# Optimization experiments

Measured on AMD Instinct MI355X. Metric: run time of the kernel, lower is better.

## Reference

```python
import jax, jax.numpy as jnp
import numpy as np

B = 262144
IN = 12
HID = 256
OUT = 12


def setup_inputs() -> dict:
    key = jax.random.key(0)
    ks = jax.random.split(key, 7)
    def lin(k, fan_in, fan_out):
        kw, kb = jax.random.split(k)
        bound = 1.0 / np.sqrt(fan_in)
        W = jax.random.uniform(kw, (fan_in, fan_out), jnp.float32, -bound, bound)
        b = jax.random.uniform(kb, (fan_out,), jnp.float32, -bound, bound)
        return W, b
    W1, b1 = lin(ks[0], IN, HID)
    W2, b2 = lin(ks[1], HID, HID)
    W3, b3 = lin(ks[2], HID, OUT)
    inp = jax.random.normal(ks[3], (B, IN), jnp.float32)
    return {"inp": inp, "W1": W1, "b1": b1, "W2": W2, "b2": b2, "W3": W3, "b3": b3}


def _forward(inp, W1, b1, W2, b2, W3, b3):
    h = jax.nn.relu(inp @ W1 + b1)
    h = jax.nn.relu(h @ W2 + b2)
    x = h @ W3 + b3  # [B, 12]

    pos = jnp.tanh(x[:, 0:3])
    vel = jnp.tanh(x[:, 3:6])
    pts = jax.nn.sigmoid(x[:, 6:7])
    clus = jnp.tanh(x[:, 7:10])
    sun = jnp.tanh(x[:, 10:12])

    # position clipped to unit sphere
    dist = jnp.linalg.norm(pos, axis=1, keepdims=True)  # [B,1]
    pos_c = jnp.where(dist > 1.0, pos / dist, pos)

    # inspected points: over-estimates set to 1, under-estimates set to previous
    prev = inp[:, 6:7]
    pts_c = jnp.where(pts > 1.0, 1.0, pts)
    pts_c = jnp.where(pts < prev, prev, pts_c)

    # cluster: push away from deputy if moving toward it, then clip to unit sphere
    delta = clus - inp[:, 7:10]
    deputy = inp[:, 0:3] - inp[:, 7:10]
    nd = deputy / jnp.linalg.norm(deputy, axis=1, keepdims=True)
    dd = jnp.einsum('ij,ij->i', delta, deputy)[:, None]  # [B,1]
    offset = jnp.where(dd > 0.0, clus - nd, clus)
    cdist = jnp.linalg.norm(offset, axis=1, keepdims=True)
    # NOTE: non-exceeding rows keep the ORIGINAL tanh prediction (torch semantics)
    clus_c = jnp.where(cdist > 1.0, offset / cdist, clus)

    # sun angle projected onto unit circle
    sun_c = sun / jnp.linalg.norm(sun, axis=1, keepdims=True)

    return jnp.concatenate([pos_c, vel, pts_c, clus_c, sun_c], axis=1)


def reference(inp, W1, b1, W2, b2, W3, b3):
    return _forward(inp, W1, b1, W2, b2, W3, b3)
```

## Files before the change

### kernel.cpp

```cpp
#include <hip/hip_runtime.h>
#include <math.h>

#define NIN 12
#define HID 256
#define NOUT 12
#define BM 64
#define NBLK (262144 / BM)

typedef _Float16 f16;
typedef f16 f16x8 __attribute__((ext_vector_type(8)));
typedef float f32x4 __attribute__((ext_vector_type(4)));

__device__ __forceinline__ void gll16(const void* g, void* l) {
    __builtin_amdgcn_global_load_lds(
        (const __attribute__((address_space(1))) unsigned int*)g,
        (__attribute__((address_space(3))) unsigned int*)l, 16, 0, 0);
}

__global__ void prep_w2(const float* __restrict__ W2, f16* __restrict__ w2p) {
    const int e = (blockIdx.x * 256 + threadIdx.x) * 4;
    const int k = e >> 8, col0 = e & 255;
    const float4 w = *(const float4*)(W2 + k * HID + col0);
    const int s = k >> 5, lgw = (k >> 3) & 3, j = k & 7;
    #pragma unroll
    for (int q = 0; q < 4; ++q) {
        const float v = ((const float*)&w)[q];
        const f16 hi = (f16)v;
        const f16 lo = (f16)(v - (float)hi);
        const int c = col0 + q, ct = c >> 4, cc = c & 15, l = (lgw << 4) | cc;
        w2p[(size_t)(((s*2 + 0)*16 + ct)*64 + l)*8 + j] = hi;
        w2p[(size_t)(((s*2 + 1)*16 + ct)*64 + l)*8 + j] = lo;
    }
}

__global__ __launch_bounds__(256, 3)
void mlp_main(const float* __restrict__ inp, const float* __restrict__ W1,
              const float* __restrict__ b1, const float* __restrict__ W2,
              const float* __restrict__ b2, const float* __restrict__ W3,
              const float* __restrict__ b3, const f16* __restrict__ w2p,
              float* __restrict__ out)
{
    __shared__ __align__(16) unsigned char smem[48896];
    __shared__ int nflag;
    __shared__ int flaglist[16];

    f16*   Bl   = (f16*)smem;
    float* W3s  = (float*)(smem + 32768);
    float* b2s  = (float*)(smem + 45056);
    float* h1f  = (float*)(smem + 46080);
    float* h2f  = (float*)(smem + 47104);
    float* psum = (float*)(smem + 48128);

    const int t    = threadIdx.x;
    const int lane = t & 63;
    const int wid  = t >> 6;
    const int cl   = lane & 15;
    const int lg   = lane >> 4;
    const int row0 = blockIdx.x * BM;

    if (t == 0) nflag = 0;

    {
        const char* w3c = (const char*)W3;
        #pragma unroll
        for (int i = 0; i < 3; ++i) {
            const int off = (wid*3 + i) * 1024;
            gll16(w3c + off + lane*16, (char*)W3s + off);
        }
        if (wid == 0) gll16((const char*)b2 + lane*16, (char*)b2s);
    }

    const int myrow = row0 + wid*16 + cl;
    float xin[12];
    {
        const f32x4* ip = (const f32x4*)(inp + (size_t)myrow * NIN);
        const f32x4 a = ip[0], b = ip[1], c = ip[2];
        xin[0]=a.x; xin[1]=a.y; xin[2]=a.z; xin[3]=a.w;
        xin[4]=b.x; xin[5]=b.y; xin[6]=b.z; xin[7]=b.w;
        xin[8]=c.x; xin[9]=c.y; xin[10]=c.z; xin[11]=c.w;
    }

    f32x4 acc[16];
    {
        const f32x4 zero = {0.f, 0.f, 0.f, 0.f};
        #pragma unroll
        for (int ct = 0; ct < 16; ++ct) acc[ct] = zero;
    }
    for (int s = 0; s < 8; ++s) {
        __syncthreads();
        const char* src = (const char*)w2p + (size_t)s * 32768;
        #pragma unroll
        for (int i = 0; i < 8; ++i) {
            const int off = (i*4 + wid) * 1024;
            gll16(src + off + lane*16, (char*)Bl + off);
        }
        const int k0 = 32*s + 8*lg;
        float a0[8];
        {
            const f32x4 bb0 = *(const f32x4*)(b1 + k0);
            const f32x4 bb1 = *(const f32x4*)(b1 + k0 + 4);
            a0[0]=bb0.x; a0[1]=bb0.y; a0[2]=bb0.z; a0[3]=bb0.w;
            a0[4]=bb1.x; a0[5]=bb1.y; a0[6]=bb1.z; a0[7]=bb1.w;
        }
        #pragma unroll
        for (int m = 0; m < 12; ++m) {
            const float xm = xin[m];
            const f32x4 w0 = *(const f32x4*)(W1 + m*HID + k0);
            const f32x4 w1 = *(const f32x4*)(W1 + m*HID + k0 + 4);
            a0[0] = fmaf(xm, w0.x, a0[0]); a0[1] = fmaf(xm, w0.y, a0[1]);
            a0[2] = fmaf(xm, w0.z, a0[2]); a0[3] = fmaf(xm, w0.w, a0[3]);
            a0[4] = fmaf(xm, w1.x, a0[4]); a0[5] = fmaf(xm, w1.y, a0[5]);
            a0[6] = fmaf(xm, w1.z, a0[6]); a0[7] = fmaf(xm, w1.w, a0[7]);
        }
        f16x8 ahi, alo;
        #pragma unroll
        for (int j = 0; j < 8; ++j) {
            const float h = fmaxf(a0[j], 0.f);
            const f16 hi = (f16)h;
            ahi[j] = hi;
            alo[j] = (f16)(h - (float)hi);
        }
        asm volatile("s_waitcnt vmcnt(0)" ::: "memory");
        __syncthreads();
        #pragma unroll
        for (int ct = 0; ct < 16; ++ct) {
            const f16x8 bhi = *(const f16x8*)((const char*)Bl + (size_t)(( 0 + ct)*64 + lane)*16);
            const f16x8 blo = *(const f16x8*)((const char*)Bl + (size_t)((16 + ct)*64 + lane)*16);
            acc[ct] = __builtin_amdgcn_mfma_f32_16x16x32_f16(ahi, bhi, acc[ct], 0, 0, 0);
            acc[ct] = __builtin_amdgcn_mfma_f32_16x16x32_f16(ahi, blo, acc[ct], 0, 0, 0);
            acc[ct] = __builtin_amdgcn_mfma_f32_16x16x32_f16(alo, bhi, acc[ct], 0, 0, 0);
        }
    }

    float x[12];
    {
        float part[4][8];
        #pragma unroll
        for (int q = 0; q < 4; ++q)
            #pragma unroll
            for (int jj = 0; jj < 8; ++jj) part[q][jj] = 0.f;

        #pragma unroll
        for (int ct = 0; ct < 16; ++ct) {
            const int col = ct*16 + cl;
            const float bv = b2s[col];
            const f32x4 w3a = *(const f32x4*)(W3s + col*12);
            const f32x4 w3b = *(const f32x4*)(W3s + col*12 + 4);
            #pragma unroll
            for (int q = 0; q < 4; ++q) {
                const float h2 = fmaxf(acc[ct][q] + bv, 0.f);
                part[q][0] = fmaf(h2, w3a.x, part[q][0]);
                part[q][1] = fmaf(h2, w3a.y, part[q][1]);
                part[q][2] = fmaf(h2, w3a.z, part[q][2]);
                part[q][3] = fmaf(h2, w3a.w, part[q][3]);
                part[q][4] = fmaf(h2, w3b.x, part[q][4]);
                part[q][5] = fmaf(h2, w3b.y, part[q][5]);
                part[q][6] = fmaf(h2, w3b.z, part[q][6]);
                part[q][7] = fmaf(h2, w3b.w, part[q][7]);
            }
        }
        #pragma unroll
        for (int m = 1; m < 16; m <<= 1) {
            #pragma unroll
            for (int q = 0; q < 4; ++q)
                #pragma unroll
                for (int jj = 0; jj < 8; ++jj)
                    part[q][jj] += __shfl_xor(part[q][jj], m);
        }
        if (cl < 4) {
            #pragma unroll
            for (int jj = 0; jj < 8; ++jj) x[jj] = part[cl][jj];
        }
    }
    {
        float part[4][4];
        #pragma unroll
        for (int q = 0; q < 4; ++q)
            #pragma unroll
            for (int jj = 0; jj < 4; ++jj) part[q][jj] = 0.f;

        #pragma unroll
        for (int ct = 0; ct < 16; ++ct) {
            const int col = ct*16 + cl;
            const float bv = b2s[col];
            const f32x4 w3c = *(const f32x4*)(W3s + col*12 + 8);
            #pragma unroll
            for (int q = 0; q < 4; ++q) {
                const float h2 = fmaxf(acc[ct][q] + bv, 0.f);
                part[q][0] = fmaf(h2, w3c.x, part[q][0]);
                part[q][1] = fmaf(h2, w3c.y, part[q][1]);
                part[q][2] = fmaf(h2, w3c.z, part[q][2]);
                part[q][3] = fmaf(h2, w3c.w, part[q][3]);
            }
        }
        #pragma unroll
        for (int m = 1; m < 16; m <<= 1) {
            #pragma unroll
            for (int q = 0; q < 4; ++q)
                #pragma unroll
                for (int jj = 0; jj < 4; ++jj)
                    part[q][jj] += __shfl_xor(part[q][jj], m);
        }
        if (cl < 4) {
            #pragma unroll
            for (int jj = 0; jj < 4; ++jj) x[8 + jj] = part[cl][jj];
        }
    }

    if (cl < 4) {
        const int R = wid*16 + 4*lg + cl;
        const int grow = row0 + R;
        #pragma unroll
        for (int jj = 0; jj < 12; ++jj) x[jj] += b3[jj];

        const f32x4* ip = (const f32x4*)(inp + (size_t)grow * NIN);
        const f32x4 iA = ip[0], iB = ip[1], iC = ip[2];
        const float in0=iA.x, in1=iA.y, in2=iA.z, in6=iB.z, in7=iB.w, in8=iC.x, in9=iC.y;

        const float pos0=tanhf(x[0]), pos1=tanhf(x[1]), pos2=tanhf(x[2]);
        const float vel0=tanhf(x[3]), vel1=tanhf(x[4]), vel2=tanhf(x[5]);
        const float pts = 1.f/(1.f+expf(-x[6]));
        const float cl0=tanhf(x[7]), cl1=tanhf(x[8]), cl2=tanhf(x[9]);
        const float sn0=tanhf(x[10]), sn1=tanhf(x[11]);

        const float dist = sqrtf(pos0*pos0 + pos1*pos1 + pos2*pos2);
        float pc0=pos0, pc1=pos1, pc2=pos2;
        if (dist > 1.0f) { pc0 = pos0/dist; pc1 = pos1/dist; pc2 = pos2/dist; }

        const float prev = in6;
        float pts_c = (pts > 1.0f) ? 1.0f : pts;
        pts_c = (pts < prev) ? prev : pts_c;

        const float de0 = cl0-in7, de1 = cl1-in8, de2 = cl2-in9;
        const float dp0 = in0-in7, dp1 = in1-in8, dp2 = in2-in9;
        const float dpn = sqrtf(dp0*dp0 + dp1*dp1 + dp2*dp2);
        const float nd0 = dp0/dpn, nd1 = dp1/dpn, nd2 = dp2/dpn;
        const float dd  = de0*dp0 + de1*dp1 + de2*dp2;
        float off0, off1, off2;
        if (dd > 0.0f) { off0 = cl0-nd0; off1 = cl1-nd1; off2 = cl2-nd2; }
        else           { off0 = cl0;     off1 = cl1;     off2 = cl2;     }
        const float cdist = sqrtf(off0*off0 + off1*off1 + off2*off2);
        float cc0, cc1, cc2;
        if (cdist > 1.0f) { cc0 = off0/cdist; cc1 = off1/cdist; cc2 = off2/cdist; }
        else              { cc0 = cl0;        cc1 = cl1;        cc2 = cl2;        }

        const float snn = sqrtf(sn0*sn0 + sn1*sn1);
        const float sc0 = sn0/snn, sc1 = sn1/snn;

        if (fabsf(dd) < 2e-4f || (dd > 0.f && fabsf(cdist - 1.f) < 2e-4f)) {
            const int slot = atomicAdd(&nflag, 1);
            if (slot < 16) flaglist[slot] = R;
        }

        f32x4* dst = (f32x4*)(out + (size_t)grow * NOUT);
        f32x4 o0 = {pc0, pc1, pc2, vel0};
        f32x4 o1 = {vel1, vel2, pts_c, cc0};
        f32x4 o2 = {cc1, cc2, sc0, sc1};
        dst[0] = o0; dst[1] = o1; dst[2] = o2;
    }
    __syncthreads();

    const int nf = (nflag < 16) ? nflag : 16;
    for (int f = 0; f < nf; ++f) {
        const int grow = row0 + flaglist[f];
        {
            float a = b1[t];
            const float* xr = inp + (size_t)grow * NIN;
            #pragma unroll
            for (int m = 0; m < 12; ++m) a = fmaf(xr[m], W1[m*HID + t], a);
            h1f[t] = fmaxf(a, 0.f);
        }
        __syncthreads();
        {
            float a = b2[t];
            for (int k = 0; k < HID; ++k) a = fmaf(h1f[k], W2[k*HID + t], a);
            h2f[t] = fmaxf(a, 0.f);
        }
        __syncthreads();
        if (t < 12*16) {
            const int jj = t >> 4, seg = t & 15;
            float a = 0.f;
            #pragma unroll
            for (int u = 0; u < 16; ++u) a = fmaf(h2f[seg*16 + u], W3[(seg*16 + u)*NOUT + jj], a);
            psum[jj*16 + seg] = a;
        }
        __syncthreads();
        if (t == 0) {
            float xx[12];
            #pragma unroll
            for (int jj = 0; jj < 12; ++jj) {
                float sacc = b3[jj];
                for (int g = 0; g < 16; ++g) sacc += psum[jj*16 + g];
                xx[jj] = sacc;
            }
            const float* xr = inp + (size_t)grow * NIN;
            const float in0=xr[0], in1=xr[1], in2=xr[2], in6=xr[6], in7=xr[7], in8=xr[8], in9=xr[9];
            const float pos0=tanhf(xx[0]), pos1=tanhf(xx[1]), pos2=tanhf(xx[2]);
            const float vel0=tanhf(xx[3]), vel1=tanhf(xx[4]), vel2=tanhf(xx[5]);
            const float pts = 1.f/(1.f+expf(-xx[6]));
            const float cl0=tanhf(xx[7]), cl1=tanhf(xx[8]), cl2=tanhf(xx[9]);
            const float sn0=tanhf(xx[10]), sn1=tanhf(xx[11]);
            const float dist = sqrtf(pos0*pos0 + pos1*pos1 + pos2*pos2);
            float pc0=pos0, pc1=pos1, pc2=pos2;
            if (dist > 1.0f) { pc0 = pos0/dist; pc1 = pos1/dist; pc2 = pos2/dist; }
            const float prev = in6;
            float pts_c = (pts > 1.0f) ? 1.0f : pts;
            pts_c = (pts < prev) ? prev : pts_c;
            const float de0 = cl0-in7, de1 = cl1-in8, de2 = cl2-in9;
            const float dp0 = in0-in7, dp1 = in1-in8, dp2 = in2-in9;
            const float dpn = sqrtf(dp0*dp0 + dp1*dp1 + dp2*dp2);
            const float nd0 = dp0/dpn, nd1 = dp1/dpn, nd2 = dp2/dpn;
            const float dd  = de0*dp0 + de1*dp1 + de2*dp2;
            float off0, off1, off2;
            if (dd > 0.0f) { off0 = cl0-nd0; off1 = cl1-nd1; off2 = cl2-nd2; }
            else           { off0 = cl0;     off1 = cl1;     off2 = cl2;     }
            const float cdist = sqrtf(off0*off0 + off1*off1 + off2*off2);
            float cc0, cc1, cc2;
            if (cdist > 1.0f) { cc0 = off0/cdist; cc1 = off1/cdist; cc2 = off2/cdist; }
            else              { cc0 = cl0;        cc1 = cl1;        cc2 = cl2;        }
            const float snn = sqrtf(sn0*sn0 + sn1*sn1);
            const float sc0 = sn0/snn, sc1 = sn1/snn;
            float* dst = out + (size_t)grow * NOUT;
            dst[0]=pc0; dst[1]=pc1; dst[2]=pc2; dst[3]=vel0; dst[4]=vel1; dst[5]=vel2;
            dst[6]=pts_c; dst[7]=cc0; dst[8]=cc1; dst[9]=cc2; dst[10]=sc0; dst[11]=sc1;
        }
        __syncthreads();
    }
}

extern "C" void kernel_launch(void* const* d_in, const int* in_sizes, int n_in,
                              void* d_out, int out_size, void* d_ws, size_t ws_size,
                              hipStream_t stream) {
    const float* inp = (const float*)d_in[0];
    const float* W1  = (const float*)d_in[1];
    const float* b1  = (const float*)d_in[2];
    const float* W2  = (const float*)d_in[3];
    const float* b2  = (const float*)d_in[4];
    const float* W3  = (const float*)d_in[5];
    const float* b3  = (const float*)d_in[6];
    float* out = (float*)d_out;
    f16* w2p = (f16*)d_ws;

    hipLaunchKernelGGL(prep_w2, dim3(64), dim3(256), 0, stream, W2, w2p);
    hipLaunchKernelGGL(mlp_main, dim3(NBLK), dim3(256), 0, stream,
                       inp, W1, b1, W2, b2, W3, b3, (const f16*)w2p, out);
}
```

Before: 254.0 us.

## Load W2 fragments directly from global memory instead of staging through LDS

```diff
diff --git a/kernel.cpp b/kernel.cpp
--- a/kernel.cpp
+++ b/kernel.cpp
@@ -15,6 +15,14 @@
     __builtin_amdgcn_global_load_lds(
         (const __attribute__((address_space(1))) unsigned int*)g,
         (__attribute__((address_space(3))) unsigned int*)l, 16, 0, 0);
+}
+
+__device__ __forceinline__ float fast_tanh(float x) {
+    const float e = exp2f(x * 2.88539008177793f);
+    return 1.0f - 2.0f / (e + 1.0f);
+}
+__device__ __forceinline__ float fast_sigmoid(float x) {
+    return 1.0f / (1.0f + exp2f(-x * 1.44269504088896f));
 }
 
 __global__ void prep_w2(const float* __restrict__ W2, f16* __restrict__ w2p) {
@@ -33,23 +41,22 @@
     }
 }
 
-__global__ __launch_bounds__(256, 3)
+__global__ __launch_bounds__(256, 2)
 void mlp_main(const float* __restrict__ inp, const float* __restrict__ W1,
               const float* __restrict__ b1, const float* __restrict__ W2,
               const float* __restrict__ b2, const float* __restrict__ W3,
               const float* __restrict__ b3, const f16* __restrict__ w2p,
               float* __restrict__ out)
 {
-    __shared__ __align__(16) unsigned char smem[48896];
+    __shared__ __align__(16) unsigned char smem[16128];
     __shared__ int nflag;
     __shared__ int flaglist[16];
 
-    f16*   Bl   = (f16*)smem;
-    float* W3s  = (float*)(smem + 32768);
-    float* b2s  = (float*)(smem + 45056);
-    float* h1f  = (float*)(smem + 46080);
-    float* h2f  = (float*)(smem + 47104);
-    float* psum = (float*)(smem + 48128);
+    float* W3s  = (float*)smem;
+    float* b2s  = (float*)(smem + 12288);
+    float* h1f  = (float*)(smem + 13312);
+    float* h2f  = (float*)(smem + 14336);
+    float* psum = (float*)(smem + 15360);
 
     const int t    = threadIdx.x;
     const int lane = t & 63;
@@ -65,9 +72,9 @@
         #pragma unroll
         for (int i = 0; i < 3; ++i) {
             const int off = (wid*3 + i) * 1024;
-            gll16(w3c + off + lane*16, (char*)W3s + off);
-        }
-        if (wid == 0) gll16((const char*)b2 + lane*16, (char*)b2s);
+            gll16(w3c + off + lane*16, smem + off);
+        }
+        if (wid == 0) gll16((const char*)b2 + lane*16, smem + 12288);
     }
 
     const int myrow = row0 + wid*16 + cl;
@@ -86,14 +93,8 @@
         #pragma unroll
         for (int ct = 0; ct < 16; ++ct) acc[ct] = zero;
     }
+    #pragma unroll
     for (int s = 0; s < 8; ++s) {
-        __syncthreads();
-        const char* src = (const char*)w2p + (size_t)s * 32768;
-        #pragma unroll
-        for (int i = 0; i < 8; ++i) {
-            const int off = (i*4 + wid) * 1024;
-            gll16(src + off + lane*16, (char*)Bl + off);
-        }
         const int k0 = 32*s + 8*lg;
         float a0[8];
         {
@@ -120,17 +121,20 @@
             ahi[j] = hi;
             alo[j] = (f16)(h - (float)hi);
         }
-        asm volatile("s_waitcnt vmcnt(0)" ::: "memory");
-        __syncthreads();
+
+        const f16* bfr = w2p + (size_t)s * 16384;
         #pragma unroll
         for (int ct = 0; ct < 16; ++ct) {
-            const f16x8 bhi = *(const f16x8*)((const char*)Bl + (size_t)(( 0 + ct)*64 + lane)*16);
-            const f16x8 blo = *(const f16x8*)((const char*)Bl + (size_t)((16 + ct)*64 + lane)*16);
+            const f16x8 bhi = *(const f16x8*)(bfr + (size_t)(( 0 + ct)*64 + lane)*8);
+            const f16x8 blo = *(const f16x8*)(bfr + (size_t)((16 + ct)*64 + lane)*8);
             acc[ct] = __builtin_amdgcn_mfma_f32_16x16x32_f16(ahi, bhi, acc[ct], 0, 0, 0);
             acc[ct] = __builtin_amdgcn_mfma_f32_16x16x32_f16(ahi, blo, acc[ct], 0, 0, 0);
             acc[ct] = __builtin_amdgcn_mfma_f32_16x16x32_f16(alo, bhi, acc[ct], 0, 0, 0);
         }
     }
+
+    asm volatile("s_waitcnt vmcnt(0)" ::: "memory");
+    __syncthreads();
 
     float x[12];
     {
@@ -160,13 +164,12 @@
             }
         }
         #pragma unroll
-        for (int m = 1; m < 16; m <<= 1) {
+        for (int m = 1; m < 16; m <<= 1)
             #pragma unroll
             for (int q = 0; q < 4; ++q)
                 #pragma unroll
                 for (int jj = 0; jj < 8; ++jj)
                     part[q][jj] += __shfl_xor(part[q][jj], m);
-        }
         if (cl < 4) {
             #pragma unroll
             for (int jj = 0; jj < 8; ++jj) x[jj] = part[cl][jj];
@@ -194,13 +197,12 @@
             }
         }
         #pragma unroll
-        for (int m = 1; m < 16; m <<= 1) {
+        for (int m = 1; m < 16; m <<= 1)
             #pragma unroll
             for (int q = 0; q < 4; ++q)
                 #pragma unroll
                 for (int jj = 0; jj < 4; ++jj)
                     part[q][jj] += __shfl_xor(part[q][jj], m);
-        }
         if (cl < 4) {
             #pragma unroll
             for (int jj = 0; jj < 4; ++jj) x[8 + jj] = part[cl][jj];
@@ -217,11 +219,11 @@
         const f32x4 iA = ip[0], iB = ip[1], iC = ip[2];
         const float in0=iA.x, in1=iA.y, in2=iA.z, in6=iB.z, in7=iB.w, in8=iC.x, in9=iC.y;
 
-        const float pos0=tanhf(x[0]), pos1=tanhf(x[1]), pos2=tanhf(x[2]);
-        const float vel0=tanhf(x[3]), vel1=tanhf(x[4]), vel2=tanhf(x[5]);
-        const float pts = 1.f/(1.f+expf(-x[6]));
-        const float cl0=tanhf(x[7]), cl1=tanhf(x[8]), cl2=tanhf(x[9]);
-        const float sn0=tanhf(x[10]), sn1=tanhf(x[11]);
+        const float pos0=fast_tanh(x[0]), pos1=fast_tanh(x[1]), pos2=fast_tanh(x[2]);
+        const float vel0=fast_tanh(x[3]), vel1=fast_tanh(x[4]), vel2=fast_tanh(x[5]);
+        const float pts = fast_sigmoid(x[6]);
+        const float cl0=fast_tanh(x[7]), cl1=fast_tanh(x[8]), cl2=fast_tanh(x[9]);
+        const float sn0=fast_tanh(x[10]), sn1=fast_tanh(x[11]);
 
         const float dist = sqrtf(pos0*pos0 + pos1*pos1 + pos2*pos2);
         float pc0=pos0, pc1=pos1, pc2=pos2;
```

New measurement: 370.6 us. +45.9%, slower.
